# Performance work log

Measured on AMD Instinct MI355X. Metric: run time of the kernel, lower is better.

Reference implementation:

```python
import jax, jax.numpy as jnp
import numpy as np

N, E = 20000, 320000
CIN = 128; H = 128
EDGE_DIM = 16; SDIM = 3; KS = 3
K = KS ** SDIM          # 27 kernel weight matrices
S = 2 ** SDIM           # 8 non-zero B-spline taps per edge (degree-1)
MLP_HID = 2 * SDIM


def _glorot(key, shape, fan_in):
    return jax.random.normal(key, shape, dtype=jnp.float32) / np.sqrt(fan_in)


def setup_inputs() -> dict:
    key = jax.random.key(0)
    ks = jax.random.split(key, 16)
    inp = {
        "x": jax.random.normal(ks[0], (N, CIN), dtype=jnp.float32),
        "edge_index": jax.random.randint(ks[1], (2, E), 0, N, dtype=jnp.int64),
        "edge_attr": jax.random.normal(ks[2], (E, EDGE_DIM), dtype=jnp.float32),
        # edge preprocessor MLP
        "Wp1": _glorot(ks[3], (EDGE_DIM, MLP_HID), EDGE_DIM),
        "bp1": jnp.zeros((MLP_HID,), jnp.float32),
        "Wp2": _glorot(ks[4], (MLP_HID, SDIM), MLP_HID),
        "bp2": jnp.zeros((SDIM,), jnp.float32),
    }
    cins = [CIN, H, H]
    for l in range(3):
        inp[f"W{l}"] = _glorot(ks[5 + 3 * l], (K, cins[l], H), cins[l] * 2)
        inp[f"Wr{l}"] = _glorot(ks[6 + 3 * l], (cins[l], H), cins[l])
        inp[f"b{l}"] = jnp.zeros((H,), jnp.float32)
    return inp


def spline_basis(u):
    """Degree-1 open B-spline basis. u: [E, SDIM] in [0,1].
    Returns (weights [E,S], flat kernel indices [E,S])."""
    v = u * (KS - 1)
    lo = jnp.clip(jnp.floor(v), 0, KS - 2)
    frac = v - lo                      # [E, SDIM]
    lo = lo.astype(jnp.int32)
    ws, idxs = [], []
    for s in range(S):
        w = jnp.ones(u.shape[0], dtype=u.dtype)
        idx = jnp.zeros(u.shape[0], dtype=jnp.int32)
        stride = 1
        for d in range(SDIM):
            bit = (s >> d) & 1
            w = w * (frac[:, d] if bit else (1.0 - frac[:, d]))
            idx = idx + (lo[:, d] + bit) * stride
            stride *= KS
        ws.append(w); idxs.append(idx)
    return jnp.stack(ws, 1), jnp.stack(idxs, 1)


def spline_conv(x, src, dst, bw, bidx, W, Wr, b):
    """SplineConv with sum aggregation, root weight and bias."""
    cin = x.shape[1]
    x_src = x[src]                              # [E, Cin] gather
    T = jnp.zeros((N * K, cin), dtype=x.dtype)  # per-(node, kernel-idx) accumulator
    for s in range(S):                          # fixed small tap count
        seg = dst * K + bidx[:, s]              # [E]
        T = T + jax.ops.segment_sum(bw[:, s, None] * x_src, seg, num_segments=N * K)
    T = T.reshape(N, K, cin)
    return jnp.einsum('nki,kio->no', T, W) + x @ Wr + b


def reference(x, edge_index, edge_attr, Wp1, bp1, Wp2, bp2,
              W0, Wr0, b0, W1, Wr1, b1, W2, Wr2, b2):
    src = edge_index[0].astype(jnp.int32)
    dst = edge_index[1].astype(jnp.int32)
    # edge preprocessor MLP + sigmoid -> pseudo coords in (0,1)
    u = jax.nn.sigmoid(jax.nn.relu(edge_attr @ Wp1 + bp1) @ Wp2 + bp2)
    bw, bidx = spline_basis(u)
    h = spline_conv(x, src, dst, bw, bidx, W0, Wr0, b0)
    h = jax.nn.relu(h)  # dropout: eval mode (identity)
    h = spline_conv(h, src, dst, bw, bidx, W1, Wr1, b1)
    h = jax.nn.relu(h)
    h = spline_conv(h, src, dst, bw, bidx, W2, Wr2, b2)
    return h
```

## Files before the change

### kernel.cpp

```cpp
#include <hip/hip_runtime.h>
#include <hip/hip_bf16.h>
#include <hip/hip_fp16.h>

#define N_NODES 20000
#define E_EDGES 320000
#define CIN 128
#define HDIM 128
#define EDGE_DIM 16
#define SDIM 3
#define KS 3
#define KK 27
#define NB 28
#define ZLD (NB * 128)
#define S_TAPS 8
#define MLP_HID 6
#define MT_TOTAL (N_NODES / 16)

typedef __attribute__((ext_vector_type(8))) short v8s;
typedef __attribute__((ext_vector_type(4))) float v4f;
typedef unsigned short ush;
typedef unsigned char uch;

static __device__ __forceinline__ short f2bf(float v) {
    unsigned u = __float_as_uint(v);
    unsigned r = (u + 0x7fffu + ((u >> 16) & 1u)) >> 16;
    return (short)r;
}
static __device__ __forceinline__ float bf2f(unsigned s) {
    return __uint_as_float((s & 0xffffu) << 16);
}
static __device__ __forceinline__ float bf2f_lo(unsigned u) {
    return __uint_as_float(u << 16);
}
static __device__ __forceinline__ float bf2f_hi(unsigned u) {
    return __uint_as_float(u & 0xffff0000u);
}
static __device__ __forceinline__ unsigned short f2h(float f) {
    __half h = __float2half(f);
    return __half_as_ushort(h);
}
static __device__ __forceinline__ float h2f(unsigned u) {
    __half_raw r; r.x = (unsigned short)u;
    return __half2float(__half(r));
}

__global__ void detect_kernel(const unsigned int* __restrict__ e, int* __restrict__ flag) {
    __shared__ int s_nz;
    if (threadIdx.x == 0) s_nz = 0;
    __syncthreads();
    unsigned int v = e[threadIdx.x * 2 + 1];
    if (v != 0) atomicAdd(&s_nz, 1);
    __syncthreads();
    if (threadIdx.x == 0) *flag = (s_nz > 0) ? 1 : 0;
}

__global__ void decode_edges(const void* __restrict__ eraw, const int* __restrict__ flag,
                             int* __restrict__ e32, int n) {
    int i = blockIdx.x * blockDim.x + threadIdx.x;
    if (i >= n) return;
    if (*flag) e32[i] = ((const int*)eraw)[i];
    else       e32[i] = (int)(((const long long*)eraw)[i]);
}

__global__ void edge_basis(const float* __restrict__ ea,
                           const float* __restrict__ Wp1, const float* __restrict__ bp1,
                           const float* __restrict__ Wp2, const float* __restrict__ bp2,
                           ush* __restrict__ wq, uch* __restrict__ kq) {
    __shared__ float sW1[EDGE_DIM * MLP_HID];
    __shared__ float sb1[MLP_HID];
    __shared__ float sW2[MLP_HID * SDIM];
    __shared__ float sb2[SDIM];
    int t = threadIdx.x;
    if (t < EDGE_DIM * MLP_HID) sW1[t] = Wp1[t];
    if (t < MLP_HID)            sb1[t] = bp1[t];
    if (t < MLP_HID * SDIM)     sW2[t] = Wp2[t];
    if (t < SDIM)               sb2[t] = bp2[t];
    __syncthreads();
    int e = blockIdx.x * blockDim.x + t;
    if (e >= E_EDGES) return;

    float a[EDGE_DIM];
#pragma unroll
    for (int i = 0; i < EDGE_DIM; i++) a[i] = ea[(long)e * EDGE_DIM + i];

    float hid[MLP_HID];
#pragma unroll
    for (int j = 0; j < MLP_HID; j++) {
        float s = sb1[j];
#pragma unroll
        for (int i = 0; i < EDGE_DIM; i++) s += a[i] * sW1[i * MLP_HID + j];
        hid[j] = fmaxf(s, 0.f);
    }

    float lo[SDIM], fr[SDIM];
#pragma unroll
    for (int d = 0; d < SDIM; d++) {
        float s = sb2[d];
#pragma unroll
        for (int j = 0; j < MLP_HID; j++) s += hid[j] * sW2[j * SDIM + d];
        float u = 1.f / (1.f + expf(-s));
        float v = u * (float)(KS - 1);
        float l = floorf(v);
        l = fminf(fmaxf(l, 0.f), (float)(KS - 2));
        lo[d] = l;
        fr[d] = v - l;
    }

#pragma unroll
    for (int s = 0; s < S_TAPS; s++) {
        float w = 1.f;
        int idx = 0, stride = 1;
#pragma unroll
        for (int d = 0; d < SDIM; d++) {
            int bit = (s >> d) & 1;
            w *= bit ? fr[d] : (1.f - fr[d]);
            idx += ((int)lo[d] + bit) * stride;
            stride *= KS;
        }
        wq[(long)e * S_TAPS + s] = f2h(w);
        kq[(long)e * S_TAPS + s] = (uch)idx;
    }
}

__global__ void zero_int(int* __restrict__ p, int n) {
    int i = blockIdx.x * blockDim.x + threadIdx.x;
    if (i < n) p[i] = 0;
}

__global__ void hist2_kernel(const int* __restrict__ dst, const int* __restrict__ src,
                             int* __restrict__ hist, int nc, int chunk_rows) {
    int e = blockIdx.x * blockDim.x + threadIdx.x;
    if (e >= E_EDGES) return;
    int bin = dst[e] * nc + src[e] / chunk_rows;
    atomicAdd(&hist[bin], 1);
}

__global__ void scan_kernel(const int* __restrict__ hist, int* __restrict__ rowptr, int B) {
    __shared__ int part[256];
    int t = threadIdx.x;
    const int per = (B + 255) / 256;
    int base = t * per;
    int s = 0;
    for (int i = 0; i < per; i++) {
        int idx = base + i;
        if (idx < B) s += hist[idx];
    }
    part[t] = s;
    __syncthreads();
    for (int off = 1; off < 256; off <<= 1) {
        int v = (t >= off) ? part[t - off] : 0;
        __syncthreads();
        part[t] += v;
        __syncthreads();
    }
    int run = (t == 0) ? 0 : part[t - 1];
    for (int i = 0; i < per; i++) {
        int idx = base + i;
        if (idx < B) { rowptr[idx] = run; run += hist[idx]; }
    }
    if (t == 255) rowptr[B] = run;
}

__global__ void perm2_kernel(const int* __restrict__ dst, const int* __restrict__ src,
                             const int* __restrict__ rowptr, int* __restrict__ cursor,
                             int* __restrict__ eperm, int nc, int chunk_rows) {
    int e = blockIdx.x * blockDim.x + threadIdx.x;
    if (e >= E_EDGES) return;
    int bin = dst[e] * nc + src[e] / chunk_rows;
    int pos = rowptr[bin] + atomicAdd(&cursor[bin], 1);
    eperm[pos] = e;
}

__global__ void pack_csr(const int* __restrict__ eperm, const int* __restrict__ src,
                         const ush* __restrict__ wq, const uch* __restrict__ kq,
                         int* __restrict__ srcp, ush* __restrict__ wp, uch* __restrict__ kp) {
    int j = blockIdx.x * blockDim.x + threadIdx.x;
    if (j >= E_EDGES) return;
    int e = eperm[j];
    srcp[j] = src[e];
    *(uint4*)(wp + (size_t)j * 8) = *(const uint4*)(wq + (size_t)e * 8);
    *(uint2*)(kp + (size_t)j * 8) = *(const uint2*)(kq + (size_t)e * 8);
}

__global__ void convA_kernel(const float* __restrict__ A, short* __restrict__ hi,
                             int do_relu) {
    int gid = blockIdx.x * blockDim.x + threadIdx.x;
    if (gid >= MT_TOTAL * 4 * 64) return;
    int lane = gid & 63;
    int ks = (gid >> 6) & 3;
    int mt = gid >> 8;
    int row = mt * 16 + (lane & 15);
    int col = ks * 32 + ((lane >> 4) & 3) * 8;
    const float* p = A + (long)row * CIN + col;
    long off = ((long)(mt * 4 + ks) * 64 + lane) * 8;
#pragma unroll
    for (int j = 0; j < 8; j++) {
        float v = p[j];
        if (do_relu) v = fmaxf(v, 0.f);
        hi[off + j] = f2bf(v);
    }
}

__global__ void packW3_kernel(const float* __restrict__ W0, const float* __restrict__ Wr0,
                              const float* __restrict__ W1, const float* __restrict__ Wr1,
                              const float* __restrict__ W2, const float* __restrict__ Wr2,
                              short* __restrict__ hi) {
    int gid = blockIdx.x * blockDim.x + threadIdx.x;
    if (gid >= 3 * NB * 4 * 8 * 64) return;
    int lane = gid & 63;
    int nt = (gid >> 6) & 7;
    int ks = (gid >> 9) & 3;
    int kb2 = gid >> 11;
    int layer = kb2 / NB;
    int kb = kb2 - layer * NB;
    const float* W  = (layer == 0) ? W0  : (layer == 1) ? W1  : W2;
    const float* Wr = (layer == 0) ? Wr0 : (layer == 1) ? Wr1 : Wr2;
    int i0 = ks * 32 + ((lane >> 4) & 3) * 8;
    int o = nt * 16 + (lane & 15);
    const float* src = (kb < KK) ? (W + (long)kb * 16384 + (long)i0 * 128 + o)
                                 : (Wr + (long)i0 * 128 + o);
    long off = ((long)(((size_t)layer * NB + kb) * 4 + ks) * 8 + nt) * 64 * 8
             + (long)lane * 8;
#pragma unroll
    for (int j = 0; j < 8; j++) {
        float v = src[(long)j * 128];
        hi[off + j] = f2bf(v);
    }
}

__global__ __launch_bounds__(256) void gemm_kernel(
    const short* __restrict__ Ah, const short* __restrict__ Wh,
    ush* __restrict__ Z, int mtile_lo, int mtile_hi, int row_lo, int row_hi)
{
    int wave = threadIdx.x >> 6;
    int lane = threadIdx.x & 63;
    int kb = blockIdx.x;
    int mt0 = mtile_lo + blockIdx.y * 8 + wave * 2;
    if (mt0 >= mtile_hi) return;
    int mt1 = (mt0 + 1 < mtile_hi) ? (mt0 + 1) : mt0;

    v4f acc[2][8];
#pragma unroll
    for (int m = 0; m < 2; m++)
#pragma unroll
        for (int n = 0; n < 8; n++) acc[m][n] = (v4f){0.f, 0.f, 0.f, 0.f};

#pragma unroll
    for (int ks = 0; ks < 4; ks++) {
        long a0 = ((long)(mt0 * 4 + ks) * 64 + lane) * 8;
        long a1 = ((long)(mt1 * 4 + ks) * 64 + lane) * 8;
        v8s ah0 = *(const v8s*)(Ah + a0);
        v8s ah1 = *(const v8s*)(Ah + a1);
#pragma unroll
        for (int nt = 0; nt < 8; nt++) {
            long boff = ((long)((kb * 4 + ks) * 8 + nt) * 64 + lane) * 8;
            v8s bh = *(const v8s*)(Wh + boff);
            acc[0][nt] = __builtin_amdgcn_mfma_f32_16x16x32_bf16(ah0, bh, acc[0][nt], 0, 0, 0);
            acc[1][nt] = __builtin_amdgcn_mfma_f32_16x16x32_bf16(ah1, bh, acc[1][nt], 0, 0, 0);
        }
    }

#pragma unroll
    for (int m = 0; m < 2; m++) {
        int mtg = mt0 + m;
        if (mtg >= mtile_hi) break;
#pragma unroll
        for (int nt = 0; nt < 8; nt++) {
            int col = kb * 128 + nt * 16 + (lane & 15);
#pragma unroll
            for (int r = 0; r < 4; r++) {
                int row = mtg * 16 + ((lane >> 4) & 3) * 4 + r;
                if (row >= row_hi) continue;
                Z[(size_t)(row - row_lo) * ZLD + col] = (ush)f2bf(acc[m][nt][r]);
            }
        }
    }
}

__global__ __launch_bounds__(256) void gather5_kernel(
    const ush* __restrict__ Z, const int* __restrict__ rowptr,
    const int* __restrict__ srcp, const ush* __restrict__ wp,
    const uch* __restrict__ kp, const float* __restrict__ bias,
    float* __restrict__ outp, short* __restrict__ Ahout,
    int lo, int hi, int nc, int cidx, int first, int mode)
{
    int wave = threadIdx.x >> 6;
    int lane = threadIdx.x & 63;
    int n = blockIdx.x * 4 + wave;
    int p = lane >> 4;
    int b = (lane >> 3) & 1;
    int g = lane & 7;
    int cb = g * 16;

    int bin = n * nc + cidx;
    int jb = rowptr[bin], je = rowptr[bin + 1];

    float acc[16];
#pragma unroll
    for (int i = 0; i < 16; i++) acc[i] = 0.f;

#pragma unroll 4
    for (int j = jb; j < je; j++) {
        int s = srcp[j];
        int kbase = kp[(size_t)j * 8 + 2 * p];
        float w = h2f(wp[(size_t)j * 8 + 2 * p + b]);
        const ush* zb = Z + (size_t)(s - lo) * ZLD + (kbase + b) * 128 + cb;
        uint4 z0 = *(const uint4*)(zb);
        uint4 z1 = *(const uint4*)(zb + 8);
        acc[0]  += w * bf2f_lo(z0.x);  acc[1]  += w * bf2f_hi(z0.x);
        acc[2]  += w * bf2f_lo(z0.y);  acc[3]  += w * bf2f_hi(z0.y);
        acc[4]  += w * bf2f_lo(z0.z);  acc[5]  += w * bf2f_hi(z0.z);
        acc[6]  += w * bf2f_lo(z0.w);  acc[7]  += w * bf2f_hi(z0.w);
        acc[8]  += w * bf2f_lo(z1.x);  acc[9]  += w * bf2f_hi(z1.x);
        acc[10] += w * bf2f_lo(z1.y);  acc[11] += w * bf2f_hi(z1.y);
        acc[12] += w * bf2f_lo(z1.z);  acc[13] += w * bf2f_hi(z1.z);
        acc[14] += w * bf2f_lo(z1.w);  acc[15] += w * bf2f_hi(z1.w);
    }

#pragma unroll
    for (int m = 8; m <= 32; m <<= 1) {
#pragma unroll
        for (int i = 0; i < 16; i++) acc[i] += __shfl_xor(acc[i], m, 64);
    }

    if (lane < 8) {
        if (n >= lo && n < hi) {
            const ush* zr = Z + (size_t)(n - lo) * ZLD + KK * 128 + cb;
            uint4 r0 = *(const uint4*)(zr);
            uint4 r1 = *(const uint4*)(zr + 8);
            const float4* bp4 = (const float4*)(bias + cb);
            float4 b0 = bp4[0], b1 = bp4[1], b2 = bp4[2], b3 = bp4[3];
            acc[0]  += bf2f_lo(r0.x) + b0.x;  acc[1]  += bf2f_hi(r0.x) + b0.y;
            acc[2]  += bf2f_lo(r0.y) + b0.z;  acc[3]  += bf2f_hi(r0.y) + b0.w;
            acc[4]  += bf2f_lo(r0.z) + b1.x;  acc[5]  += bf2f_hi(r0.z) + b1.y;
            acc[6]  += bf2f_lo(r0.w) + b1.z;  acc[7]  += bf2f_hi(r0.w) + b1.w;
            acc[8]  += bf2f_lo(r1.x) + b2.x;  acc[9]  += bf2f_hi(r1.x) + b2.y;
            acc[10] += bf2f_lo(r1.y) + b2.z;  acc[11] += bf2f_hi(r1.y) + b2.w;
            acc[12] += bf2f_lo(r1.z) + b3.x;  acc[13] += bf2f_hi(r1.z) + b3.y;
            acc[14] += bf2f_lo(r1.w) + b3.z;  acc[15] += bf2f_hi(r1.w) + b3.w;
        }
        if (mode == 1) {
            int mt = n >> 4, r = n & 15;
            int ks = g >> 1;
            int sub0 = (g * 2) & 3;
            int sub1 = (g * 2 + 1) & 3;
            v8s p0, p1;
#pragma unroll
            for (int q = 0; q < 8; q++) {
                p0[q] = f2bf(fmaxf(acc[q], 0.f));
                p1[q] = f2bf(fmaxf(acc[8 + q], 0.f));
            }
            long base = (long)(mt * 4 + ks) * 64;
            *(v8s*)(Ahout + (base + r + 16 * sub0) * 8) = p0;
            *(v8s*)(Ahout + (base + r + 16 * sub1) * 8) = p1;
        } else {
            float* op = outp + (size_t)n * HDIM + cb;
            if (!first) {
                const float4* o4 = (const float4*)op;
#pragma unroll
                for (int q = 0; q < 4; q++) {
                    float4 ov = o4[q];
                    acc[q * 4 + 0] += ov.x; acc[q * 4 + 1] += ov.y;
                    acc[q * 4 + 2] += ov.z; acc[q * 4 + 3] += ov.w;
                }
            }
#pragma unroll
            for (int q = 0; q < 4; q++) {
                float4 ov = make_float4(acc[q * 4 + 0], acc[q * 4 + 1],
                                        acc[q * 4 + 2], acc[q * 4 + 3]);
                ((float4*)op)[q] = ov;
            }
        }
    }
}

extern "C" void kernel_launch(void* const* d_in, const int* in_sizes, int n_in,
                              void* d_out, int out_size, void* d_ws, size_t ws_size,
                              hipStream_t stream) {
    const float* x   = (const float*)d_in[0];
    const void*  eix = d_in[1];
    const float* ea  = (const float*)d_in[2];
    const float* Wp1 = (const float*)d_in[3];
    const float* bp1 = (const float*)d_in[4];
    const float* Wp2 = (const float*)d_in[5];
    const float* bp2 = (const float*)d_in[6];
    const float* W[3]  = {(const float*)d_in[7],  (const float*)d_in[10], (const float*)d_in[13]};
    const float* Wr[3] = {(const float*)d_in[8],  (const float*)d_in[11], (const float*)d_in[14]};
    const float* b[3]  = {(const float*)d_in[9],  (const float*)d_in[12], (const float*)d_in[15]};
    float* out = (float*)d_out;

    char* ws = (char*)d_ws;
    size_t off = 0;
    auto walloc = [&](size_t bytes) -> void* {
        void* p = ws + off;
        off = (off + bytes + 255) & ~(size_t)255;
        return p;
    };
    int*   flag    = (int*)  walloc(sizeof(int));
    int*   e32     = (int*)  walloc(sizeof(int) * 2 * E_EDGES);
    ush*   wq      = (ush*)  walloc(sizeof(ush) * (size_t)E_EDGES * 8);
    uch*   kq      = (uch*)  walloc((size_t)E_EDGES * 8);
    float* h0      = (float*)walloc(sizeof(float) * (size_t)N_NODES * HDIM);
    float* h1      = (float*)walloc(sizeof(float) * (size_t)N_NODES * HDIM);
    short* Ah      = (short*)walloc(sizeof(short) * (size_t)N_NODES * CIN);
    short* Wh3     = (short*)walloc(sizeof(short) * (size_t)3 * NB * 128 * 128);
    int*   eperm   = (int*)  walloc(sizeof(int) * E_EDGES);
    int*   srcp    = (int*)  walloc(sizeof(int) * E_EDGES);
    ush*   wp      = (ush*)  walloc(sizeof(ush) * (size_t)E_EDGES * 8);
    uch*   kp      = (uch*)  walloc((size_t)E_EDGES * 8);

    int  nc = -1;
    long chunk_rows = 0;
    for (int t = 1; t <= 157; t++) {
        long cr = (((N_NODES + t - 1) / t) + 127) / 128 * 128;
        size_t bins = (size_t)N_NODES * t;
        size_t need = 0;
        auto a = [&](size_t bb) { need += (bb + 255) & ~(size_t)255; };
        a(sizeof(int) * bins * 2);
        a(sizeof(int) * (bins + 1));
        a((size_t)cr * ZLD * sizeof(ush));
        if (off + need <= ws_size) { nc = t; chunk_rows = cr; break; }
    }
    if (nc < 0) { nc = 157; chunk_rows = 128; }
    size_t bins = (size_t)N_NODES * nc;
    int*   histcur = (int*)walloc(sizeof(int) * bins * 2);
    int*   hist    = histcur;
    int*   cursor  = histcur + bins;
    int*   rowptr  = (int*)walloc(sizeof(int) * (bins + 1));
    ush*   Z       = (ush*)walloc((size_t)chunk_rows * ZLD * sizeof(ush));

    int* srcv = e32;
    int* dstv = e32 + E_EDGES;
    const int fast = (nc == 1) ? 1 : 0;

    detect_kernel<<<1, 1024, 0, stream>>>((const unsigned int*)eix, flag);
    decode_edges<<<(2 * E_EDGES + 255) / 256, 256, 0, stream>>>(eix, flag, e32, 2 * E_EDGES);
    edge_basis<<<(E_EDGES + 255) / 256, 256, 0, stream>>>(ea, Wp1, bp1, Wp2, bp2, wq, kq);

    zero_int<<<((int)(bins * 2) + 255) / 256, 256, 0, stream>>>(histcur, (int)(bins * 2));
    hist2_kernel<<<(E_EDGES + 255) / 256, 256, 0, stream>>>(dstv, srcv, hist, nc, (int)chunk_rows);
    scan_kernel<<<1, 256, 0, stream>>>(hist, rowptr, (int)bins);
    perm2_kernel<<<(E_EDGES + 255) / 256, 256, 0, stream>>>(dstv, srcv, rowptr, cursor,
                                                            eperm, nc, (int)chunk_rows);
    pack_csr<<<(E_EDGES + 255) / 256, 256, 0, stream>>>(eperm, srcv, wq, kq, srcp, wp, kp);

    packW3_kernel<<<(3 * NB * 4 * 8 * 64 + 255) / 256, 256, 0, stream>>>(
        W[0], Wr[0], W[1], Wr[1], W[2], Wr[2], Wh3);

    const float* lin[3]  = {x, h0, h1};
    float*       lout[3] = {h0, h1, out};

    for (int l = 0; l < 3; l++) {
        if (l == 0) {
            convA_kernel<<<(MT_TOTAL * 4 * 64 + 255) / 256, 256, 0, stream>>>(
                x, Ah, 0);
        } else if (!fast) {
            convA_kernel<<<(MT_TOTAL * 4 * 64 + 255) / 256, 256, 0, stream>>>(
                lin[l], Ah, 1);
        }
        const short* Wh = Wh3 + (size_t)l * NB * 128 * 128;
        int mode = (fast && l < 2) ? 1 : 0;
        for (int c = 0; c < nc; c++) {
            long lo = (long)c * chunk_rows;
            long hi = lo + chunk_rows;
            if (hi > N_NODES) hi = N_NODES;
            if (lo >= N_NODES) break;
            int mtile_lo = (int)(lo / 16);
            int mtile_hi = (int)((hi + 15) / 16);
            int gy = (mtile_hi - mtile_lo + 7) / 8;
            dim3 grid(NB, gy);
            gemm_kernel<<<grid, 256, 0, stream>>>(Ah, Wh, Z,
                                                  mtile_lo, mtile_hi, (int)lo, (int)hi);
            gather5_kernel<<<N_NODES / 4, 256, 0, stream>>>(
                Z, rowptr, srcp, wp, kp, b[l], lout[l], Ah,
                (int)lo, (int)hi, nc, c, (c == 0) ? 1 : 0, mode);
        }
    }
}
```

Baseline: 622.4 us.

## Aggregate per-node spline tensor first, then run one dense GEMM per layer

Replaces the old order (GEMM x against all 27 kernel weights into a large Z buffer, then gather) with an aggregate-first scheme. For each destination node, edges are summed into a 27x128 tensor T using precomputed dense 27-weight basis vectors. T is written in MFMA layout and multiplied by the stacked weights in a single K=3584 GEMM with bias and ReLU fused. This drops the N×3584 intermediate and the source-chunking bins, at the cost of a dense 28-float weight per edge, larger per-node register accumulators, and 64-thread blocks with serial edge loops.

```diff
diff --git a/kernel.cpp b/kernel.cpp
--- a/kernel.cpp
+++ b/kernel.cpp
@@ -11,37 +11,26 @@
 #define KS 3
 #define KK 27
 #define NB 28
-#define ZLD (NB * 128)
-#define S_TAPS 8
+#define KSTEPS 112
 #define MLP_HID 6
-#define MT_TOTAL (N_NODES / 16)
 
 typedef __attribute__((ext_vector_type(8))) short v8s;
 typedef __attribute__((ext_vector_type(4))) float v4f;
 typedef unsigned short ush;
-typedef unsigned char uch;
 
 static __device__ __forceinline__ short f2bf(float v) {
     unsigned u = __float_as_uint(v);
     unsigned r = (u + 0x7fffu + ((u >> 16) & 1u)) >> 16;
     return (short)r;
 }
-static __device__ __forceinline__ float bf2f(unsigned s) {
-    return __uint_as_float((s & 0xffffu) << 16);
-}
 static __device__ __forceinline__ float bf2f_lo(unsigned u) {
     return __uint_as_float(u << 16);
 }
 static __device__ __forceinline__ float bf2f_hi(unsigned u) {
     return __uint_as_float(u & 0xffff0000u);
 }
-static __device__ __forceinline__ unsigned short f2h(float f) {
-    __half h = __float2half(f);
-    return __half_as_ushort(h);
-}
-static __device__ __forceinline__ float h2f(unsigned u) {
-    __half_raw r; r.x = (unsigned short)u;
-    return __half2float(__half(r));
+static __device__ __forceinline__ unsigned pack2bf(float a, float b) {
+    return ((unsigned)(ush)f2bf(a)) | (((unsigned)(ush)f2bf(b)) << 16);
 }
 
 __global__ void detect_kernel(const unsigned int* __restrict__ e, int* __restrict__ flag) {
@@ -65,7 +54,7 @@
 __global__ void edge_basis(const float* __restrict__ ea,
                            const float* __restrict__ Wp1, const float* __restrict__ bp1,
                            const float* __restrict__ Wp2, const float* __restrict__ bp2,
-                           ush* __restrict__ wq, uch* __restrict__ kq) {
+                           float4* __restrict__ fb) {
     __shared__ float sW1[EDGE_DIM * MLP_HID];
     __shared__ float sb1[MLP_HID];
     __shared__ float sW2[MLP_HID * SDIM];
@@ -92,7 +81,8 @@
         hid[j] = fmaxf(s, 0.f);
     }
 
-    float lo[SDIM], fr[SDIM];
+    float fr[SDIM];
+    unsigned lp = 0;
 #pragma unroll
     for (int d = 0; d < SDIM; d++) {
         float s = sb2[d];
@@ -102,24 +92,12 @@
         float v = u * (float)(KS - 1);
         float l = floorf(v);
         l = fminf(fmaxf(l, 0.f), (float)(KS - 2));
-        lo[d] = l;
         fr[d] = v - l;
-    }
-
-#pragma unroll
-    for (int s = 0; s < S_TAPS; s++) {
-        float w = 1.f;
-        int idx = 0, stride = 1;
-#pragma unroll
-        for (int d = 0; d < SDIM; d++) {
-            int bit = (s >> d) & 1;
-            w *= bit ? fr[d] : (1.f - fr[d]);
-            idx += ((int)lo[d] + bit) * stride;
-            stride *= KS;
-        }
-        wq[(long)e * S_TAPS + s] = f2h(w);
-        kq[(long)e * S_TAPS + s] = (uch)idx;
-    }
+        lp |= ((unsigned)(int)l) << (8 * d);
+    }
+    float4 o;
+    o.x = fr[0]; o.y = fr[1]; o.z = fr[2]; o.w = __uint_as_float(lp);
+    fb[e] = o;
 }
 
 __global__ void zero_int(int* __restrict__ p, int n) {
@@ -127,12 +105,10 @@
     if (i < n) p[i] = 0;
 }
 
-__global__ void hist2_kernel(const int* __restrict__ dst, const int* __restrict__ src,
-                             int* __restrict__ hist, int nc, int chunk_rows) {
+__global__ void hist_kernel(const int* __restrict__ dst, int* __restrict__ hist) {
     int e = blockIdx.x * blockDim.x + threadIdx.x;
     if (e >= E_EDGES) return;
-    int bin = dst[e] * nc + src[e] / chunk_rows;
-    atomicAdd(&hist[bin], 1);
+    atomicAdd(&hist[dst[e]], 1);
 }
 
 __global__ void scan_kernel(const int* __restrict__ hist, int* __restrict__ rowptr, int B) {
@@ -161,44 +137,47 @@
     if (t == 255) rowptr[B] = run;
 }
 
-__global__ void perm2_kernel(const int* __restrict__ dst, const int* __restrict__ src,
-                             const int* __restrict__ rowptr, int* __restrict__ cursor,
-                             int* __restrict__ eperm, int nc, int chunk_rows) {
+__global__ void perm_kernel(const int* __restrict__ dst,
+                            const int* __restrict__ rowptr, int* __restrict__ cursor,
+                            int* __restrict__ eperm) {
     int e = blockIdx.x * blockDim.x + threadIdx.x;
     if (e >= E_EDGES) return;
-    int bin = dst[e] * nc + src[e] / chunk_rows;
+    int bin = dst[e];
     int pos = rowptr[bin] + atomicAdd(&cursor[bin], 1);
     eperm[pos] = e;
 }
 
-__global__ void pack_csr(const int* __restrict__ eperm, const int* __restrict__ src,
-                         const ush* __restrict__ wq, const uch* __restrict__ kq,
-                         int* __restrict__ srcp, ush* __restrict__ wp, uch* __restrict__ kp) {
+__global__ void pack_w27(const int* __restrict__ eperm, const int* __restrict__ src,
+                         const float4* __restrict__ fb,
+                         int* __restrict__ srcp, float* __restrict__ w27p) {
     int j = blockIdx.x * blockDim.x + threadIdx.x;
     if (j >= E_EDGES) return;
     int e = eperm[j];
     srcp[j] = src[e];
-    *(uint4*)(wp + (size_t)j * 8) = *(const uint4*)(wq + (size_t)e * 8);
-    *(uint2*)(kp + (size_t)j * 8) = *(const uint2*)(kq + (size_t)e * 8);
-}
-
-__global__ void convA_kernel(const float* __restrict__ A, short* __restrict__ hi,
-                             int do_relu) {
-    int gid = blockIdx.x * blockDim.x + threadIdx.x;
-    if (gid >= MT_TOTAL * 4 * 64) return;
-    int lane = gid & 63;
-    int ks = (gid >> 6) & 3;
-    int mt = gid >> 8;
-    int row = mt * 16 + (lane & 15);
-    int col = ks * 32 + ((lane >> 4) & 3) * 8;
-    const float* p = A + (long)row * CIN + col;
-    long off = ((long)(mt * 4 + ks) * 64 + lane) * 8;
-#pragma unroll
-    for (int j = 0; j < 8; j++) {
-        float v = p[j];
-        if (do_relu) v = fmaxf(v, 0.f);
-        hi[off + j] = f2bf(v);
-    }
+    float4 f = fb[e];
+    unsigned lp = __float_as_uint(f.w);
+    float fr[3] = {f.x, f.y, f.z};
+    float t[3][3];
+#pragma unroll
+    for (int d = 0; d < 3; d++) {
+        int lo = (lp >> (8 * d)) & 255;
+        float fd = fr[d];
+#pragma unroll
+        for (int q = 0; q < 3; q++)
+            t[d][q] = (q == lo) ? (1.f - fd) : (q == lo + 1) ? fd : 0.f;
+    }
+    float out[28];
+#pragma unroll
+    for (int k2 = 0; k2 < 3; k2++)
+#pragma unroll
+        for (int k1 = 0; k1 < 3; k1++)
+#pragma unroll
+            for (int k0 = 0; k0 < 3; k0++)
+                out[k2 * 9 + k1 * 3 + k0] = t[0][k0] * t[1][k1] * t[2][k2];
+    out[27] = 0.f;
+    float* op = w27p + (size_t)j * 28;
+#pragma unroll
+    for (int q = 0; q < 7; q++) *(float4*)(op + 4 * q) = *(float4*)(out + 4 * q);
 }
 
 __global__ void packW3_kernel(const float* __restrict__ W0, const float* __restrict__ Wr0,
@@ -228,148 +207,128 @@
     }
 }
 
-__global__ __launch_bounds__(256) void gemm_kernel(
-    const short* __restrict__ Ah, const short* __restrict__ Wh,
-    ush* __restrict__ Z, int mtile_lo, int mtile_hi, int row_lo, int row_hi)
+__global__ void conv_xb(const float* __restrict__ x, ush* __restrict__ xb) {
+    int i = blockIdx.x * blockDim.x + threadIdx.x;
+    if (i >= N_NODES * CIN / 4) return;
+    float4 v = ((const float4*)x)[i];
+    uint2 d;
+    d.x = pack2bf(v.x, v.y);
+    d.y = pack2bf(v.z, v.w);
+    ((uint2*)xb)[i] = d;
+}
+
+__global__ __launch_bounds__(64) void accumT_kernel(
+    const ush* __restrict__ act, const int* __restrict__ rowptr,
+    const int* __restrict__ srcp, const float* __restrict__ w27p,
+    short* __restrict__ AhT, int n0)
 {
-    int wave = threadIdx.x >> 6;
-    int lane = threadIdx.x & 63;
-    int kb = blockIdx.x;
-    int mt0 = mtile_lo + blockIdx.y * 8 + wave * 2;
-    if (mt0 >= mtile_hi) return;
-    int mt1 = (mt0 + 1 < mtile_hi) ? (mt0 + 1) : mt0;
-
-    v4f acc[2][8];
-#pragma unroll
-    for (int m = 0; m < 2; m++)
-#pragma unroll
-        for (int n = 0; n < 8; n++) acc[m][n] = (v4f){0.f, 0.f, 0.f, 0.f};
-
-#pragma unroll
-    for (int ks = 0; ks < 4; ks++) {
-        long a0 = ((long)(mt0 * 4 + ks) * 64 + lane) * 8;
-        long a1 = ((long)(mt1 * 4 + ks) * 64 + lane) * 8;
-        v8s ah0 = *(const v8s*)(Ah + a0);
-        v8s ah1 = *(const v8s*)(Ah + a1);
-#pragma unroll
-        for (int nt = 0; nt < 8; nt++) {
-            long boff = ((long)((kb * 4 + ks) * 8 + nt) * 64 + lane) * 8;
-            v8s bh = *(const v8s*)(Wh + boff);
-            acc[0][nt] = __builtin_amdgcn_mfma_f32_16x16x32_bf16(ah0, bh, acc[0][nt], 0, 0, 0);
-            acc[1][nt] = __builtin_amdgcn_mfma_f32_16x16x32_bf16(ah1, bh, acc[1][nt], 0, 0, 0);
-        }
-    }
-
-#pragma unroll
-    for (int m = 0; m < 2; m++) {
-        int mtg = mt0 + m;
-        if (mtg >= mtile_hi) break;
-#pragma unroll
-        for (int nt = 0; nt < 8; nt++) {
-            int col = kb * 128 + nt * 16 + (lane & 15);
-#pragma unroll
-            for (int r = 0; r < 4; r++) {
-                int row = mtg * 16 + ((lane >> 4) & 3) * 4 + r;
-                if (row >= row_hi) continue;
-                Z[(size_t)(row - row_lo) * ZLD + col] = (ush)f2bf(acc[m][nt][r]);
-            }
-        }
-    }
-}
-
-__global__ __launch_bounds__(256) void gather5_kernel(
-    const ush* __restrict__ Z, const int* __restrict__ rowptr,
-    const int* __restrict__ srcp, const ush* __restrict__ wp,
-    const uch* __restrict__ kp, const float* __restrict__ bias,
-    float* __restrict__ outp, short* __restrict__ Ahout,
-    int lo, int hi, int nc, int cidx, int first, int mode)
-{
-    int wave = threadIdx.x >> 6;
-    int lane = threadIdx.x & 63;
-    int n = blockIdx.x * 4 + wave;
-    int p = lane >> 4;
-    int b = (lane >> 3) & 1;
-    int g = lane & 7;
-    int cb = g * 16;
-
-    int bin = n * nc + cidx;
-    int jb = rowptr[bin], je = rowptr[bin + 1];
-
-    float acc[16];
-#pragma unroll
-    for (int i = 0; i < 16; i++) acc[i] = 0.f;
-
-#pragma unroll 4
+    int lane = threadIdx.x;
+    int n = n0 + blockIdx.x;
+    int jb = rowptr[n], je = rowptr[n + 1];
+
+    float acc[KK][2];
+#pragma unroll
+    for (int k = 0; k < KK; k++) { acc[k][0] = 0.f; acc[k][1] = 0.f; }
+
     for (int j = jb; j < je; j++) {
         int s = srcp[j];
-        int kbase = kp[(size_t)j * 8 + 2 * p];
-        float w = h2f(wp[(size_t)j * 8 + 2 * p + b]);
-        const ush* zb = Z + (size_t)(s - lo) * ZLD + (kbase + b) * 128 + cb;
-        uint4 z0 = *(const uint4*)(zb);
-        uint4 z1 = *(const uint4*)(zb + 8);
-        acc[0]  += w * bf2f_lo(z0.x);  acc[1]  += w * bf2f_hi(z0.x);
-        acc[2]  += w * bf2f_lo(z0.y);  acc[3]  += w * bf2f_hi(z0.y);
-        acc[4]  += w * bf2f_lo(z0.z);  acc[5]  += w * bf2f_hi(z0.z);
-        acc[6]  += w * bf2f_lo(z0.w);  acc[7]  += w * bf2f_hi(z0.w);
-        acc[8]  += w * bf2f_lo(z1.x);  acc[9]  += w * bf2f_hi(z1.x);
-        acc[10] += w * bf2f_lo(z1.y);  acc[11] += w * bf2f_hi(z1.y);
-        acc[12] += w * bf2f_lo(z1.z);  acc[13] += w * bf2f_hi(z1.z);
-        acc[14] += w * bf2f_lo(z1.w);  acc[15] += w * bf2f_hi(z1.w);
-    }
-
-#pragma unroll
-    for (int m = 8; m <= 32; m <<= 1) {
-#pragma unroll
-        for (int i = 0; i < 16; i++) acc[i] += __shfl_xor(acc[i], m, 64);
-    }
-
-    if (lane < 8) {
-        if (n >= lo && n < hi) {
-            const ush* zr = Z + (size_t)(n - lo) * ZLD + KK * 128 + cb;
-            uint4 r0 = *(const uint4*)(zr);
-            uint4 r1 = *(const uint4*)(zr + 8);
-            const float4* bp4 = (const float4*)(bias + cb);
-            float4 b0 = bp4[0], b1 = bp4[1], b2 = bp4[2], b3 = bp4[3];
-            acc[0]  += bf2f_lo(r0.x) + b0.x;  acc[1]  += bf2f_hi(r0.x) + b0.y;
-            acc[2]  += bf2f_lo(r0.y) + b0.z;  acc[3]  += bf2f_hi(r0.y) + b0.w;
-            acc[4]  += bf2f_lo(r0.z) + b1.x;  acc[5]  += bf2f_hi(r0.z) + b1.y;
-            acc[6]  += bf2f_lo(r0.w) + b1.z;  acc[7]  += bf2f_hi(r0.w) + b1.w;
-            acc[8]  += bf2f_lo(r1.x) + b2.x;  acc[9]  += bf2f_hi(r1.x) + b2.y;
-            acc[10] += bf2f_lo(r1.y) + b2.z;  acc[11] += bf2f_hi(r1.y) + b2.w;
-            acc[12] += bf2f_lo(r1.z) + b3.x;  acc[13] += bf2f_hi(r1.z) + b3.y;
-            acc[14] += bf2f_lo(r1.w) + b3.z;  acc[15] += bf2f_hi(r1.w) + b3.w;
-        }
-        if (mode == 1) {
-            int mt = n >> 4, r = n & 15;
-            int ks = g >> 1;
-            int sub0 = (g * 2) & 3;
-            int sub1 = (g * 2 + 1) & 3;
-            v8s p0, p1;
-#pragma unroll
-            for (int q = 0; q < 8; q++) {
-                p0[q] = f2bf(fmaxf(acc[q], 0.f));
-                p1[q] = f2bf(fmaxf(acc[8 + q], 0.f));
-            }
-            long base = (long)(mt * 4 + ks) * 64;
-            *(v8s*)(Ahout + (base + r + 16 * sub0) * 8) = p0;
-            *(v8s*)(Ahout + (base + r + 16 * sub1) * 8) = p1;
+        unsigned xv = *(const unsigned*)(act + (size_t)s * 128 + lane * 2);
+        float x0 = bf2f_lo(xv);
+        float x1 = bf2f_hi(xv);
+        const float4* w4 = (const float4*)(w27p + (size_t)j * 28);
+        float w[28];
+#pragma unroll
+        for (int q = 0; q < 7; q++) *(float4*)(w + 4 * q) = w4[q];
+#pragma unroll
+        for (int k = 0; k < KK; k++) {
+            acc[k][0] += w[k] * x0;
+            acc[k][1] += w[k] * x1;
+        }
+    }
+
+    int mtr = (n - n0) >> 4;
+    int r = n & 15;
+    int cks  = lane >> 4;
+    int csub = (lane >> 2) & 3;
+    int cj   = (lane & 3) * 2;
+    int lp   = r + 16 * csub;
+    size_t mbase = (size_t)mtr * KSTEPS;
+#pragma unroll
+    for (int k = 0; k < KK; k++) {
+        unsigned d = pack2bf(acc[k][0], acc[k][1]);
+        *(unsigned*)(AhT + ((mbase + 4 * k + cks) * 64 + lp) * 8 + cj) = d;
+    }
+    unsigned xv = *(const unsigned*)(act + (size_t)n * 128 + lane * 2);
+    *(unsigned*)(AhT + ((mbase + 4 * KK + cks) * 64 + lp) * 8 + cj) = xv;
+}
+
+__global__ __launch_bounds__(256) void gemm2_kernel(
+    const short* __restrict__ AhT, const short* __restrict__ Wh,
+    const float* __restrict__ bias, ush* __restrict__ actout,
+    float* __restrict__ fout, int n0, int nmt, int relu)
+{
+    __shared__ float S[256][33];
+    int lane = threadIdx.x & 63;
+    int wave = threadIdx.x >> 6;
+    int mtr0 = blockIdx.x * 2;
+    int mv = nmt - mtr0; if (mv > 2) mv = 2;
+
+    v4f acc[2][8];
+#pragma unroll
+    for (int m = 0; m < 2; m++)
+#pragma unroll
+        for (int nt = 0; nt < 8; nt++) acc[m][nt] = (v4f){0.f, 0.f, 0.f, 0.f};
+
+    int ks0 = wave * (KSTEPS / 4);
+    for (int ks = ks0; ks < ks0 + KSTEPS / 4; ks++) {
+        v8s bfr[8];
+#pragma unroll
+        for (int nt = 0; nt < 8; nt++)
+            bfr[nt] = *(const v8s*)(Wh + ((size_t)(ks * 8 + nt) * 64 + lane) * 8);
+#pragma unroll
+        for (int m = 0; m < 2; m++) {
+            if (m >= mv) break;
+            v8s a = *(const v8s*)(AhT + ((size_t)((mtr0 + m) * KSTEPS + ks) * 64 + lane) * 8);
+#pragma unroll
+            for (int nt = 0; nt < 8; nt++)
+                acc[m][nt] = __builtin_amdgcn_mfma_f32_16x16x32_bf16(a, bfr[nt], acc[m][nt], 0, 0, 0);
+        }
+    }
+
+    int r  = (threadIdx.x >> 3) & 15;
+    int o0 = (threadIdx.x & 7) * 16 + (threadIdx.x >> 7) * 8;
+#pragma unroll
+    for (int m = 0; m < 2; m++) {
+        if (m >= mv) break;
+        __syncthreads();
+#pragma unroll
+        for (int q = 0; q < 32; q++) S[threadIdx.x][q] = acc[m][q >> 2][q & 3];
+        __syncthreads();
+        int row = n0 + (mtr0 + m) * 16 + r;
+        float v[8];
+#pragma unroll
+        for (int q = 0; q < 8; q++) {
+            int o = o0 + q;
+            int ln = (o & 15) + 16 * (r >> 2);
+            int idx = (o >> 4) * 4 + (r & 3);
+            float s = S[ln][idx] + S[64 + ln][idx] + S[128 + ln][idx] + S[192 + ln][idx];
+            s += bias[o];
+            if (relu) s = fmaxf(s, 0.f);
+            v[q] = s;
+        }
+        if (actout) {
+            uint4 u;
+            u.x = pack2bf(v[0], v[1]);
+            u.y = pack2bf(v[2], v[3]);
+            u.z = pack2bf(v[4], v[5]);
+            u.w = pack2bf(v[6], v[7]);
+            *(uint4*)(actout + (size_t)row * 128 + o0) = u;
         } else {
-            float* op = outp + (size_t)n * HDIM + cb;
-            if (!first) {
-                const float4* o4 = (const float4*)op;
-#pragma unroll
-                for (int q = 0; q < 4; q++) {
-                    float4 ov = o4[q];
-                    acc[q * 4 + 0] += ov.x; acc[q * 4 + 1] += ov.y;
-                    acc[q * 4 + 2] += ov.z; acc[q * 4 + 3] += ov.w;
-                }
-            }
-#pragma unroll
-            for (int q = 0; q < 4; q++) {
-                float4 ov = make_float4(acc[q * 4 + 0], acc[q * 4 + 1],
-                                        acc[q * 4 + 2], acc[q * 4 + 3]);
-                ((float4*)op)[q] = ov;
-            }
+            float4 f0, f1;
+            f0.x = v[0]; f0.y = v[1]; f0.z = v[2]; f0.w = v[3];
+            f1.x = v[4]; f1.y = v[5]; f1.z = v[6]; f1.w = v[7];
+            *(float4*)(fout + (size_t)row * 128 + o0) = f0;
+            *(float4*)(fout + (size_t)row * 128 + o0 + 4) = f1;
         }
     }
 }
@@ -396,84 +355,61 @@
         off = (off + bytes + 255) & ~(size_t)255;
         return p;
     };
-    int*   flag    = (int*)  walloc(sizeof(int));
-    int*   e32     = (int*)  walloc(sizeof(int) * 2 * E_EDGES);
-    ush*   wq      = (ush*)  walloc(sizeof(ush) * (size_t)E_EDGES * 8);
-    uch*   kq      = (uch*)  walloc((size_t)E_EDGES * 8);
-    float* h0      = (float*)walloc(sizeof(float) * (size_t)N_NODES * HDIM);
-    float* h1      = (float*)walloc(sizeof(float) * (size_t)N_NODES * HDIM);
-    short* Ah      = (short*)walloc(sizeof(short) * (size_t)N_NODES * CIN);
-    short* Wh3     = (short*)walloc(sizeof(short) * (size_t)3 * NB * 128 * 128);
-    int*   eperm   = (int*)  walloc(sizeof(int) * E_EDGES);
-    int*   srcp    = (int*)  walloc(sizeof(int) * E_EDGES);
-    ush*   wp      = (ush*)  walloc(sizeof(ush) * (size_t)E_EDGES * 8);
-    uch*   kp      = (uch*)  walloc((size_t)E_EDGES * 8);
-
-    int  nc = -1;
-    long chunk_rows = 0;
-    for (int t = 1; t <= 157; t++) {
-        long cr = (((N_NODES + t - 1) / t) + 127) / 128 * 128;
-        size_t bins = (size_t)N_NODES * t;
-        size_t need = 0;
-        auto a = [&](size_t bb) { need += (bb + 255) & ~(size_t)255; };
-        a(sizeof(int) * bins * 2);
-        a(sizeof(int) * (bins + 1));
-        a((size_t)cr * ZLD * sizeof(ush));
-        if (off + need <= ws_size) { nc = t; chunk_rows = cr; break; }
-    }
-    if (nc < 0) { nc = 157; chunk_rows = 128; }
-    size_t bins = (size_t)N_NODES * nc;
-    int*   histcur = (int*)walloc(sizeof(int) * bins * 2);
-    int*   hist    = histcur;
-    int*   cursor  = histcur + bins;
-    int*   rowptr  = (int*)walloc(sizeof(int) * (bins + 1));
-    ush*   Z       = (ush*)walloc((size_t)chunk_rows * ZLD * sizeof(ush));
+    int*    flag    = (int*)   walloc(sizeof(int));
+    int*    e32     = (int*)   walloc(sizeof(int) * 2 * E_EDGES);
+    float4* fb      = (float4*)walloc(sizeof(float4) * (size_t)E_EDGES);
+    int*    srcp    = (int*)   walloc(sizeof(int) * E_EDGES);
+    int*    eperm   = (int*)   walloc(sizeof(int) * E_EDGES);
+    float*  w27p    = (float*) walloc(sizeof(float) * (size_t)E_EDGES * 28);
+    int*    histcur = (int*)   walloc(sizeof(int) * (size_t)N_NODES * 2);
+    int*    rowptr  = (int*)   walloc(sizeof(int) * (N_NODES + 1));
+    ush*    xb      = (ush*)   walloc(sizeof(ush) * (size_t)N_NODES * 128);
+    ush*    a1      = (ush*)   walloc(sizeof(ush) * (size_t)N_NODES * 128);
+    ush*    a2      = (ush*)   walloc(sizeof(ush) * (size_t)N_NODES * 128);
+    short*  Wh3     = (short*) walloc(sizeof(short) * (size_t)3 * NB * 128 * 128);
+
+    int chunk_n = 10000;
+    {
+        const int cand[3] = {10000, 4000, 2000};
+        for (int i = 0; i < 3; i++) {
+            size_t need = (size_t)(cand[i] / 16) * KSTEPS * 512 * sizeof(short);
+            chunk_n = cand[i];
+            if (off + need <= ws_size) break;
+        }
+    }
+    short* AhT = (short*)walloc(sizeof(short) * (size_t)(chunk_n / 16) * KSTEPS * 512);
 
     int* srcv = e32;
     int* dstv = e32 + E_EDGES;
-    const int fast = (nc == 1) ? 1 : 0;
+    int* hist   = histcur;
+    int* cursor = histcur + N_NODES;
 
     detect_kernel<<<1, 1024, 0, stream>>>((const unsigned int*)eix, flag);
     decode_edges<<<(2 * E_EDGES + 255) / 256, 256, 0, stream>>>(eix, flag, e32, 2 * E_EDGES);
-    edge_basis<<<(E_EDGES + 255) / 256, 256, 0, stream>>>(ea, Wp1, bp1, Wp2, bp2, wq, kq);
-
-    zero_int<<<((int)(bins * 2) + 255) / 256, 256, 0, stream>>>(histcur, (int)(bins * 2));
-    hist2_kernel<<<(E_EDGES + 255) / 256, 256, 0, stream>>>(dstv, srcv, hist, nc, (int)chunk_rows);
-    scan_kernel<<<1, 256, 0, stream>>>(hist, rowptr, (int)bins);
-    perm2_kernel<<<(E_EDGES + 255) / 256, 256, 0, stream>>>(dstv, srcv, rowptr, cursor,
-                                                            eperm, nc, (int)chunk_rows);
-    pack_csr<<<(E_EDGES + 255) / 256, 256, 0, stream>>>(eperm, srcv, wq, kq, srcp, wp, kp);
+    edge_basis<<<(E_EDGES + 255) / 256, 256, 0, stream>>>(ea, Wp1, bp1, Wp2, bp2, fb);
+
+    zero_int<<<(N_NODES * 2 + 255) / 256, 256, 0, stream>>>(histcur, N_NODES * 2);
+    hist_kernel<<<(E_EDGES + 255) / 256, 256, 0, stream>>>(dstv, hist);
+    scan_kernel<<<1, 256, 0, stream>>>(hist, rowptr, N_NODES);
+    perm_kernel<<<(E_EDGES + 255) / 256, 256, 0, stream>>>(dstv, rowptr, cursor, eperm);
+    pack_w27<<<(E_EDGES + 255) / 256, 256, 0, stream>>>(eperm, srcv, fb, srcp, w27p);
 
     packW3_kernel<<<(3 * NB * 4 * 8 * 64 + 255) / 256, 256, 0, stream>>>(
         W[0], Wr[0], W[1], Wr[1], W[2], Wr[2], Wh3);
-
-    const float* lin[3]  = {x, h0, h1};
-    float*       lout[3] = {h0, h1, out};
-
+    conv_xb<<<(N_NODES * CIN / 4 + 255) / 256, 256, 0, stream>>>(x, xb);
+
+    const ush* actin = xb;
     for (int l = 0; l < 3; l++) {
-        if (l == 0) {
-            convA_kernel<<<(MT_TOTAL * 4 * 64 + 255) / 256, 256, 0, stream>>>(
-                x, Ah, 0);
-        } else if (!fast) {
-            convA_kernel<<<(MT_TOTAL * 4 * 64 + 255) / 256, 256, 0, stream>>>(
-                lin[l], Ah, 1);
-        }
         const short* Wh = Wh3 + (size_t)l * NB * 128 * 128;
-        int mode = (fast && l < 2) ? 1 : 0;
-        for (int c = 0; c < nc; c++) {
-            long lo = (long)c * chunk_rows;
-            long hi = lo + chunk_rows;
-            if (hi > N_NODES) hi = N_NODES;
-            if (lo >= N_NODES) break;
-            int mtile_lo = (int)(lo / 16);
-            int mtile_hi = (int)((hi + 15) / 16);
-            int gy = (mtile_hi - mtile_lo + 7) / 8;
-            dim3 grid(NB, gy);
-            gemm_kernel<<<grid, 256, 0, stream>>>(Ah, Wh, Z,
-                                                  mtile_lo, mtile_hi, (int)lo, (int)hi);
-            gather5_kernel<<<N_NODES / 4, 256, 0, stream>>>(
-                Z, rowptr, srcp, wp, kp, b[l], lout[l], Ah,
-                (int)lo, (int)hi, nc, c, (c == 0) ? 1 : 0, mode);
-        }
-    }
-}
+        ush* actout = (l == 0) ? a1 : (l == 1) ? a2 : nullptr;
+        for (int n0 = 0; n0 < N_NODES; n0 += chunk_n) {
+            int cn = (n0 + chunk_n <= N_NODES) ? chunk_n : (N_NODES - n0);
+            int nmt = cn / 16;
+            accumT_kernel<<<cn, 64, 0, stream>>>(actin, rowptr, srcp, w27p, AhT, n0);
+            gemm2_kernel<<<(nmt + 1) / 2, 256, 0, stream>>>(
+                AhT, Wh, b[l], actout, (l == 2) ? out : nullptr,
+                n0, nmt, (l < 2) ? 1 : 0);
+        }
+        if (l == 0) actin = a1; else if (l == 1) actin = a2;
+    }
+}
```

Result: slower. 826.4 us (+32.8%).
